# Performance work log

Measured on AMD Instinct MI355X. Metric: run time of the kernel, lower is better.

Reference implementation:

```python
import jax, jax.numpy as jnp
import numpy as np

N, D, G = 131072, 512, 4096
EPS = 1e-12


def setup_inputs() -> dict:
    key = jax.random.key(0)
    ks = jax.random.split(key, 8)
    scale = 0.02
    x = jax.random.normal(ks[0], (N, D), dtype=jnp.float32)
    Wf = jax.random.normal(ks[1], (D, D), dtype=jnp.float32) * scale
    bf = jax.random.normal(ks[2], (D,), dtype=jnp.float32) * scale
    Wg = jax.random.normal(ks[3], (D, D), dtype=jnp.float32) * scale
    bg = jax.random.normal(ks[4], (D,), dtype=jnp.float32) * scale
    Wh = jax.random.normal(ks[5], (D, D), dtype=jnp._float32 if False else jnp.float32) * scale
    bh = jax.random.normal(ks[6], (D,), dtype=jnp.float32) * scale
    jx = jax.random.randint(ks[7], (N,), 0, G, dtype=jnp.int64 if jax.config.jax_enable_x64 else jnp.int32)
    return {"x": x, "Wf": Wf, "bf": bf, "Wg": Wg, "bg": bg,
            "Wh": Wh, "bh": bh, "jx": jx, "num_groups": G}


def reference(x, Wf, bf, Wg, bg, Wh, bh, jx, num_groups):
    # x: [N, D]; jx: [N] group ids in [0, num_groups)
    logits = x @ Wg.T + bg            # [N, D]
    feats = x @ Wf.T + bf             # [N, D]
    # group-wise stable softmax weights along the N (group-member) axis
    gmax = jax.ops.segment_max(logits, jx, num_segments=num_groups)   # [G, D]
    expv = jnp.exp(logits - gmax[jx])                                 # [N, D]
    denom = jax.ops.segment_sum(expv, jx, num_segments=num_groups)    # [G, D]
    w = expv / (denom[jx] + EPS)                                      # [N, D]
    y = jax.ops.segment_sum(feats * w, jx, num_segments=num_groups)   # [G, D]
    out_group = y @ Wh.T + bh                                         # [G, D]
    return out_group[jx]                                              # [N, D]
```

## Files before the change

kernel.cpp:

```cpp
#include <hip/hip_runtime.h>
#include <math.h>

#define NROWS 131072
#define DD    512
#define GG    4096

typedef __attribute__((ext_vector_type(8))) short bf16x8;
typedef __attribute__((ext_vector_type(4))) float f32x4;

__device__ __forceinline__ unsigned short f2b(float f) {
    unsigned u = __float_as_uint(f);
    unsigned r = (u + 0x7FFFu + ((u >> 16) & 1u)) >> 16;
    return (unsigned short)r;
}
__device__ __forceinline__ float b2f(unsigned short h) {
    return __uint_as_float(((unsigned)h) << 16);
}

__device__ __forceinline__ void async_copy16(const void* g, void* l) {
    __builtin_amdgcn_global_load_lds(
        (const __attribute__((address_space(1))) void*)g,
        (__attribute__((address_space(3))) void*)l, 16, 0, 0);
}

__global__ __launch_bounds__(256) void k_f2b(const float* __restrict__ in,
                                             unsigned short* __restrict__ out, int n4) {
    int i = blockIdx.x * blockDim.x + threadIdx.x;
    if (i < n4) {
        float4 v = ((const float4*)in)[i];
        ushort4 o;
        o.x = f2b(v.x); o.y = f2b(v.y); o.z = f2b(v.z); o.w = f2b(v.w);
        ((ushort4*)out)[i] = o;
    }
}

__global__ void k_hist(const int* __restrict__ jx, int* __restrict__ counts, int n) {
    int i = blockIdx.x * blockDim.x + threadIdx.x;
    if (i < n) atomicAdd(&counts[jx[i]], 1);
}

__global__ __launch_bounds__(1024) void k_scan4096(const int* __restrict__ counts,
                                                   int* __restrict__ offsets) {
    __shared__ int buf[GG];
    __shared__ int part[1024];
    const int t = threadIdx.x;
    for (int i = t; i < GG; i += 1024) buf[i] = counts[i];
    __syncthreads();
    const int base = t * 4;
    int s0 = buf[base + 0];
    int s1 = s0 + buf[base + 1];
    int s2 = s1 + buf[base + 2];
    int s3 = s2 + buf[base + 3];
    part[t] = s3;
    __syncthreads();
    for (int off = 1; off < 1024; off <<= 1) {
        int v = (t >= off) ? part[t - off] : 0;
        __syncthreads();
        part[t] += v;
        __syncthreads();
    }
    int excl = (t == 0) ? 0 : part[t - 1];
    offsets[base + 0] = excl;
    offsets[base + 1] = excl + s0;
    offsets[base + 2] = excl + s1;
    offsets[base + 3] = excl + s2;
    if (t == 1023) offsets[GG] = excl + s3;
}

__global__ void k_scatter(const int* __restrict__ jx, const int* __restrict__ offsets,
                          int* __restrict__ cursor, int* __restrict__ order, int n) {
    int i = blockIdx.x * blockDim.x + threadIdx.x;
    if (i < n) {
        int g = jx[i];
        int p = atomicAdd(&cursor[g], 1);
        order[offsets[g] + p] = i;
    }
}

__global__ __launch_bounds__(256) void k_dual_gemm_mfma(
    const unsigned short* __restrict__ A,
    const unsigned short* __restrict__ B1, const float* __restrict__ bias1,
    const unsigned short* __restrict__ B2, const float* __restrict__ bias2,
    unsigned short* __restrict__ C1, unsigned short* __restrict__ C2)
{
    __shared__ short sA [8192];
    __shared__ short sB1[8192];
    __shared__ short sB2[8192];

    const int t  = threadIdx.x;
    const int w  = t >> 6;
    const int L  = t & 63;
    const int wr = w >> 1;
    const int wc = w & 1;
    const int lane15 = L & 15;
    const int q  = L >> 4;

    const int m0 = blockIdx.y << 7;
    const int d0 = blockIdx.x << 7;

    f32x4 acc1[4][4], acc2[4][4];
    const f32x4 z = {0.f, 0.f, 0.f, 0.f};
    #pragma unroll
    for (int i = 0; i < 4; ++i)
        #pragma unroll
        for (int j = 0; j < 4; ++j) { acc1[i][j] = z; acc2[i][j] = z; }

    size_t offA[4], offB[4];
    int ldsoff[4];
    #pragma unroll
    for (int j = 0; j < 4; ++j) {
        const int chunk = (j << 8) + t;
        const int row   = chunk & 127;
        const int q8    = chunk >> 7;
        offA[j]   = (size_t)(m0 + row) * DD + (q8 << 3);
        offB[j]   = (size_t)(d0 + row) * DD + (q8 << 3);
        ldsoff[j] = ((j << 8) + (w << 6)) << 3;
    }

    for (int k0 = 0; k0 < DD; k0 += 64) {
        #pragma unroll
        for (int j = 0; j < 4; ++j) {
            async_copy16(A  + offA[j] + k0, &sA [ldsoff[j]]);
            async_copy16(B1 + offB[j] + k0, &sB1[ldsoff[j]]);
            async_copy16(B2 + offB[j] + k0, &sB2[ldsoff[j]]);
        }
        __syncthreads();

        #pragma unroll
        for (int kk = 0; kk < 2; ++kk) {
            bf16x8 aF[4], bF1[4], bF2[4];
            const int kbase = ((kk << 2) + q) << 10;
            #pragma unroll
            for (int i = 0; i < 4; ++i) {
                const int rA = (wr << 6) + (i << 4) + lane15;
                aF[i] = *(const bf16x8*)&sA[kbase + (rA << 3)];
            }
            #pragma unroll
            for (int j = 0; j < 4; ++j) {
                const int rB = (wc << 6) + (j << 4) + lane15;
                const int o  = kbase + (rB << 3);
                bF1[j] = *(const bf16x8*)&sB1[o];
                bF2[j] = *(const bf16x8*)&sB2[o];
            }
            #pragma unroll
            for (int i = 0; i < 4; ++i)
                #pragma unroll
                for (int j = 0; j < 4; ++j) {
                    acc1[i][j] = __builtin_amdgcn_mfma_f32_16x16x32_bf16(aF[i], bF1[j], acc1[i][j], 0, 0, 0);
                    acc2[i][j] = __builtin_amdgcn_mfma_f32_16x16x32_bf16(aF[i], bF2[j], acc2[i][j], 0, 0, 0);
                }
        }
        __syncthreads();
    }

    #pragma unroll
    for (int j = 0; j < 4; ++j) {
        const int col = d0 + (wc << 6) + (j << 4) + lane15;
        const float b1 = bias1[col];
        const float b2 = bias2[col];
        #pragma unroll
        for (int i = 0; i < 4; ++i) {
            const int row0 = m0 + (wr << 6) + (i << 4) + (q << 2);
            #pragma unroll
            for (int r = 0; r < 4; ++r) {
                C1[(size_t)(row0 + r) * DD + col] = f2b(acc1[i][j][r] + b1);
                C2[(size_t)(row0 + r) * DD + col] = f2b(acc2[i][j][r] + b2);
            }
        }
    }
}

__global__ __launch_bounds__(256) void k_gemm_bt(
    const float* __restrict__ A,
    const float* __restrict__ B1, const float* __restrict__ bias1,
    float* __restrict__ C1)
{
    __shared__ __align__(16) float sA[16][68];
    __shared__ __align__(16) float s1[16][68];

    const int t  = threadIdx.x;
    const int tx = t & 15;
    const int ty = t >> 4;
    const int m0 = blockIdx.y << 6;
    const int d0 = blockIdx.x << 6;
    const int lr = t >> 2;
    const int lk = (t & 3) << 2;

    float acc1[4][4] = {{0.f}};

    const float* pA = A  + (size_t)(m0 + lr) * DD + lk;
    const float* p1 = B1 + (size_t)(d0 + lr) * DD + lk;

    for (int k0 = 0; k0 < DD; k0 += 16) {
        float4 av = *(const float4*)(pA + k0);
        float4 v1 = *(const float4*)(p1 + k0);
        sA[lk+0][lr]=av.x; sA[lk+1][lr]=av.y; sA[lk+2][lr]=av.z; sA[lk+3][lr]=av.w;
        s1[lk+0][lr]=v1.x; s1[lk+1][lr]=v1.y; s1[lk+2][lr]=v1.z; s1[lk+3][lr]=v1.w;
        __syncthreads();
        #pragma unroll
        for (int kk = 0; kk < 16; ++kk) {
            float4 a = *(const float4*)&sA[kk][ty << 2];
            float4 u = *(const float4*)&s1[kk][tx << 2];
            float aa[4] = {a.x, a.y, a.z, a.w};
            float uu[4] = {u.x, u.y, u.z, u.w};
            #pragma unroll
            for (int i = 0; i < 4; ++i)
                #pragma unroll
                for (int j = 0; j < 4; ++j)
                    acc1[i][j] = fmaf(aa[i], uu[j], acc1[i][j]);
        }
        __syncthreads();
    }

    const int dcol = d0 + (tx << 2);
    float4 b1v = *(const float4*)&bias1[dcol];
    #pragma unroll
    for (int i = 0; i < 4; ++i) {
        int m = m0 + (ty << 2) + i;
        float4 r1;
        r1.x = acc1[i][0] + b1v.x; r1.y = acc1[i][1] + b1v.y;
        r1.z = acc1[i][2] + b1v.z; r1.w = acc1[i][3] + b1v.w;
        *(float4*)&C1[(size_t)m * DD + dcol] = r1;
    }
}

__global__ __launch_bounds__(512) void k_group_agg(
    const unsigned short* __restrict__ logits, const unsigned short* __restrict__ feats,
    const int* __restrict__ order, const int* __restrict__ offsets,
    float* __restrict__ y)
{
    const int g = blockIdx.x;
    const int d = threadIdx.x;
    const int beg = offsets[g];
    const int end = offsets[g + 1];
    if (beg == end) { y[(size_t)g * DD + d] = 0.f; return; }

    float s = 0.f, acc = 0.f;
    for (int i = beg; i < end; ++i) {
        int n = order[i];
        float e = __expf(b2f(logits[(size_t)n * DD + d]));
        float f = b2f(feats[(size_t)n * DD + d]);
        s += e;
        acc = fmaf(f, e, acc);
    }
    y[(size_t)g * DD + d] = acc / (s + 1e-12f);
}

__global__ __launch_bounds__(256) void k_gather(
    const float* __restrict__ outg, const int* __restrict__ jx,
    float* __restrict__ out)
{
    const int i  = blockIdx.x * 256 + threadIdx.x;
    const int n  = i >> 7;
    const int d4 = i & 127;
    const int g  = jx[n];
    ((float4*)out)[i] = ((const float4*)outg)[(size_t)g * (DD / 4) + d4];
}

extern "C" void kernel_launch(void* const* d_in, const int* in_sizes, int n_in,
                              void* d_out, int out_size, void* d_ws, size_t ws_size,
                              hipStream_t stream)
{
    const float* x  = (const float*)d_in[0];
    const float* Wf = (const float*)d_in[1];
    const float* bf = (const float*)d_in[2];
    const float* Wg = (const float*)d_in[3];
    const float* bg = (const float*)d_in[4];
    const float* Wh = (const float*)d_in[5];
    const float* bh = (const float*)d_in[6];
    const int*   jx = (const int*)d_in[7];
    float* out = (float*)d_out;
    const int N = in_sizes[7];

    char* ws = (char*)d_ws;
    const size_t ND2 = (size_t)N * DD * sizeof(unsigned short);
    const size_t WD2 = (size_t)DD * DD * sizeof(unsigned short);
    const size_t GD4 = (size_t)GG * DD * sizeof(float);
    size_t off = 0;
    unsigned short* xb      = (unsigned short*)(ws + off); off += ND2;
    unsigned short* logitsb = (unsigned short*)(ws + off); off += ND2;
    unsigned short* featsb  = (unsigned short*)(ws + off); off += ND2;
    unsigned short* Wgb     = (unsigned short*)(ws + off); off += WD2;
    unsigned short* Wfb     = (unsigned short*)(ws + off); off += WD2;
    float* yv   = (float*)(ws + off); off += GD4;
    float* outg = (float*)(ws + off); off += GD4;
    int* counts  = (int*)(ws + off); off += (size_t)GG * 4;
    int* offsets = (int*)(ws + off); off += (size_t)(GG + 4) * 4;
    int* cursor  = (int*)(ws + off); off += (size_t)GG * 4;
    int* order   = (int*)(ws + off); off += (size_t)N * 4;

    hipMemsetAsync(counts, 0, (size_t)GG * 4, stream);
    hipMemsetAsync(cursor, 0, (size_t)GG * 4, stream);

    k_hist<<<N / 256, 256, 0, stream>>>(jx, counts, N);
    k_scan4096<<<1, 1024, 0, stream>>>(counts, offsets);
    k_scatter<<<N / 256, 256, 0, stream>>>(jx, offsets, cursor, order, N);

    k_f2b<<<(N * (DD / 4)) / 256, 256, 0, stream>>>(x, xb, N * (DD / 4));
    k_f2b<<<(DD * DD / 4) / 256, 256, 0, stream>>>(Wg, Wgb, DD * DD / 4);
    k_f2b<<<(DD * DD / 4) / 256, 256, 0, stream>>>(Wf, Wfb, DD * DD / 4);

    k_dual_gemm_mfma<<<dim3(DD / 128, N / 128), 256, 0, stream>>>(
        xb, Wgb, bg, Wfb, bf, logitsb, featsb);

    k_group_agg<<<GG, 512, 0, stream>>>(logitsb, featsb, order, offsets, yv);

    k_gemm_bt<<<dim3(DD / 64, GG / 64), 256, 0, stream>>>(yv, Wh, bh, outg);

    k_gather<<<(N * (DD / 4)) / 256, 256, 0, stream>>>(outg, jx, out);
}
```

Before: 1.092 ms.

## Double-buffer dual GEMM LDS, remap blocks for XCD locality, unroll group aggregation

The dual GEMM now uses two LDS buffers with K-step 32, so async global-to-LDS copies for the next slice are issued while the current slice is computed, and one barrier per iteration is removed. Block indices are remapped so blocks landing on the same XCD share nearby rows and columns, which should improve L2 reuse. The group aggregation loop is unrolled by four so several gathered loads are in flight at once. The risks are higher LDS and register use, smaller K tiles per barrier, and a hardcoded grid of GG blocks that only works for these sizes.

```diff
diff --git a/kernel.cpp b/kernel.cpp
--- a/kernel.cpp
+++ b/kernel.cpp
@@ -83,9 +83,7 @@
     const unsigned short* __restrict__ B2, const float* __restrict__ bias2,
     unsigned short* __restrict__ C1, unsigned short* __restrict__ C2)
 {
-    __shared__ short sA [8192];
-    __shared__ short sB1[8192];
-    __shared__ short sB2[8192];
+    __shared__ short lds[2][3][4096];
 
     const int t  = threadIdx.x;
     const int w  = t >> 6;
@@ -95,8 +93,10 @@
     const int lane15 = L & 15;
     const int q  = L >> 4;
 
-    const int m0 = blockIdx.y << 7;
-    const int d0 = blockIdx.x << 7;
+    const int hw      = blockIdx.x;
+    const int logical = ((hw & 7) << 9) + (hw >> 3);
+    const int m0 = (logical >> 2) << 7;
+    const int d0 = (logical & 3) << 7;
 
     f32x4 acc1[4][4], acc2[4][4];
     const f32x4 z = {0.f, 0.f, 0.f, 0.f};
@@ -105,10 +105,10 @@
         #pragma unroll
         for (int j = 0; j < 4; ++j) { acc1[i][j] = z; acc2[i][j] = z; }
 
-    size_t offA[4], offB[4];
-    int ldsoff[4];
+    size_t offA[2], offB[2];
+    int ldsoff[2];
     #pragma unroll
-    for (int j = 0; j < 4; ++j) {
+    for (int j = 0; j < 2; ++j) {
         const int chunk = (j << 8) + t;
         const int row   = chunk & 127;
         const int q8    = chunk >> 7;
@@ -117,41 +117,47 @@
         ldsoff[j] = ((j << 8) + (w << 6)) << 3;
     }
 
-    for (int k0 = 0; k0 < DD; k0 += 64) {
+    auto stage = [&](int buf, int k0) {
+        #pragma unroll
+        for (int j = 0; j < 2; ++j) {
+            async_copy16(A  + offA[j] + k0, &lds[buf][0][ldsoff[j]]);
+            async_copy16(B1 + offB[j] + k0, &lds[buf][1][ldsoff[j]]);
+            async_copy16(B2 + offB[j] + k0, &lds[buf][2][ldsoff[j]]);
+        }
+    };
+
+    auto compute = [&](int cur) {
+        const short* pA  = &lds[cur][0][0];
+        const short* pB1 = &lds[cur][1][0];
+        const short* pB2 = &lds[cur][2][0];
+        bf16x8 aF[4], bF1[4], bF2[4];
+        const int kbase = q << 10;
+        #pragma unroll
+        for (int i = 0; i < 4; ++i)
+            aF[i] = *(const bf16x8*)&pA[kbase + (((wr << 6) + (i << 4) + lane15) << 3)];
         #pragma unroll
         for (int j = 0; j < 4; ++j) {
-            async_copy16(A  + offA[j] + k0, &sA [ldsoff[j]]);
-            async_copy16(B1 + offB[j] + k0, &sB1[ldsoff[j]]);
-            async_copy16(B2 + offB[j] + k0, &sB2[ldsoff[j]]);
+            const int o = kbase + (((wc << 6) + (j << 4) + lane15) << 3);
+            bF1[j] = *(const bf16x8*)&pB1[o];
+            bF2[j] = *(const bf16x8*)&pB2[o];
         }
-        __syncthreads();
-
-        #pragma unroll
-        for (int kk = 0; kk < 2; ++kk) {
-            bf16x8 aF[4], bF1[4], bF2[4];
-            const int kbase = ((kk << 2) + q) << 10;
-            #pragma unroll
-            for (int i = 0; i < 4; ++i) {
-                const int rA = (wr << 6) + (i << 4) + lane15;
-                aF[i] = *(const bf16x8*)&sA[kbase + (rA << 3)];
-            }
+        #pragma unroll
+        for (int i = 0; i < 4; ++i)
             #pragma unroll
             for (int j = 0; j < 4; ++j) {
-                const int rB = (wc << 6) + (j << 4) + lane15;
-                const int o  = kbase + (rB << 3);
-                bF1[j] = *(const bf16x8*)&sB1[o];
-                bF2[j] = *(const bf16x8*)&sB2[o];
+                acc1[i][j] = __builtin_amdgcn_mfma_f32_16x16x32_bf16(aF[i], bF1[j], acc1[i][j], 0, 0, 0);
+                acc2[i][j] = __builtin_amdgcn_mfma_f32_16x16x32_bf16(aF[i], bF2[j], acc2[i][j], 0, 0, 0);
             }
-            #pragma unroll
-            for (int i = 0; i < 4; ++i)
-                #pragma unroll
-                for (int j = 0; j < 4; ++j) {
-                    acc1[i][j] = __builtin_amdgcn_mfma_f32_16x16x32_bf16(aF[i], bF1[j], acc1[i][j], 0, 0, 0);
-                    acc2[i][j] = __builtin_amdgcn_mfma_f32_16x16x32_bf16(aF[i], bF2[j], acc2[i][j], 0, 0, 0);
-                }
-        }
-        __syncthreads();
-    }
+    };
+
+    stage(0, 0);
+    __syncthreads();
+    for (int ks = 0; ks < 15; ++ks) {
+        stage((ks + 1) & 1, (ks + 1) << 5);
+        compute(ks & 1);
+        __syncthreads();
+    }
+    compute(1);
 
     #pragma unroll
     for (int j = 0; j < 4; ++j) {
@@ -236,10 +242,34 @@
     if (beg == end) { y[(size_t)g * DD + d] = 0.f; return; }
 
     float s = 0.f, acc = 0.f;
-    for (int i = beg; i < end; ++i) {
-        int n = order[i];
-        float e = __expf(b2f(logits[(size_t)n * DD + d]));
-        float f = b2f(feats[(size_t)n * DD + d]);
+    int i = beg;
+    for (; i + 4 <= end; i += 4) {
+        const int n0 = order[i + 0];
+        const int n1 = order[i + 1];
+        const int n2 = order[i + 2];
+        const int n3 = order[i + 3];
+        const float l0 = b2f(logits[(size_t)n0 * DD + d]);
+        const float l1 = b2f(logits[(size_t)n1 * DD + d]);
+        const float l2 = b2f(logits[(size_t)n2 * DD + d]);
+        const float l3 = b2f(logits[(size_t)n3 * DD + d]);
+        const float f0 = b2f(feats[(size_t)n0 * DD + d]);
+        const float f1 = b2f(feats[(size_t)n1 * DD + d]);
+        const float f2 = b2f(feats[(size_t)n2 * DD + d]);
+        const float f3 = b2f(feats[(size_t)n3 * DD + d]);
+        const float e0 = __expf(l0);
+        const float e1 = __expf(l1);
+        const float e2 = __expf(l2);
+        const float e3 = __expf(l3);
+        s += e0; s += e1; s += e2; s += e3;
+        acc = fmaf(f0, e0, acc);
+        acc = fmaf(f1, e1, acc);
+        acc = fmaf(f2, e2, acc);
+        acc = fmaf(f3, e3, acc);
+    }
+    for (; i < end; ++i) {
+        const int n = order[i];
+        const float e = __expf(b2f(logits[(size_t)n * DD + d]));
+        const float f = b2f(feats[(size_t)n * DD + d]);
         s += e;
         acc = fmaf(f, e, acc);
     }
@@ -300,8 +330,7 @@
     k_f2b<<<(DD * DD / 4) / 256, 256, 0, stream>>>(Wg, Wgb, DD * DD / 4);
     k_f2b<<<(DD * DD / 4) / 256, 256, 0, stream>>>(Wf, Wfb, DD * DD / 4);
 
-    k_dual_gemm_mfma<<<dim3(DD / 128, N / 128), 256, 0, stream>>>(
-        xb, Wgb, bg, Wfb, bf, logitsb, featsb);
+    k_dual_gemm_mfma<<<GG, 256, 0, stream>>>(xb, Wgb, bg, Wfb, bf, logitsb, featsb);
 
     k_group_agg<<<GG, 512, 0, stream>>>(logitsb, featsb, order, offsets, yv);
 
```

New measurement: 917.7 us. 16.0% less time.
